# Kernel tuning notes

Measured on AMD Instinct MI355X. Metric: run time of the kernel, lower is better.

## Reference

```python
import jax, jax.numpy as jnp
import numpy as np

WIN = 9  # win_size from init

def setup_inputs() -> dict:
    key = jax.random.key(0)
    ks = jax.random.split(key, 4)
    N, L, C, U = 8, 4096, 256, 256
    x = jax.random.normal(ks[0], (N, L, C), dtype=jnp.float32)
    W_qry = jax.random.normal(ks[1], (C, U), dtype=jnp.float32) * 0.05
    W_key = jax.random.normal(ks[2], (C, U), dtype=jnp.float32) * 0.05
    v = jax.random.normal(ks[3], (U,), dtype=jnp.float32) * 0.05
    b = jnp.zeros((U,), dtype=jnp.float32)
    return {"x": x, "W_qry": W_qry, "W_key": W_key, "v": v, "b": b}

def reference(x, W_qry, W_key, v, b):
    N, L, C = x.shape
    n_w = L - WIN + 1
    # sliding-window gather: idx[w, s] = w + s
    idx = jnp.arange(n_w)[:, None] + jnp.arange(WIN)[None, :]
    x_win = x[:, idx]
    x_ctr = x[:, WIN // 2 : WIN // 2 + n_w]                    # [N, n_w, C]
    key = jnp.einsum('nwsc,cu->nwsu', x_win, W_key)
    qry = jnp.einsum('nwc,cu->nwu', x_ctr, W_qry)              # [N, n_w, U]
    score = jnp.einsum('nwsu,u->nws', jnp.tanh(qry[:, :, None, :] + key + b), v)
    weight = jax.nn.softmax(score, axis=2)                     # softmax over window dim
    out = jnp.einsum('nwsc,nws->nwc', x_win, weight)           # [N, n_w, C]
    return out
```

## Files before the change

kernel.cpp:

```cpp
#include <hip/hip_runtime.h>
#include <hip/hip_bf16.h>

#define WIN   9
#define NB    8
#define LL    4096
#define CC    256
#define UU    256
#define NW    (LL - WIN + 1)
#define MROWS (NB * LL)

#define BM 128
#define BK 64

typedef unsigned short ushort;
typedef __attribute__((ext_vector_type(8))) unsigned short ushort8v;
typedef __attribute__((ext_vector_type(4))) unsigned short ushort4v;
typedef __attribute__((ext_vector_type(8))) short short8v;
typedef __attribute__((ext_vector_type(4))) float f32x4;

__device__ __forceinline__ float bf16_to_f(ushort u) {
    return __uint_as_float(((unsigned int)u) << 16);
}
__device__ __forceinline__ ushort f2bf(float f) {
    __hip_bfloat16 h = __float2bfloat16(f);
    return *reinterpret_cast<ushort*>(&h);
}
__device__ __forceinline__ float fast_tanh(float x) {
    float e = __expf(2.0f * x);
    return 1.0f - 2.0f * __builtin_amdgcn_rcpf(e + 1.0f);
}

__global__ __launch_bounds__(256) void cvt_x(const float* __restrict__ X,
                                             ushort* __restrict__ Xb) {
    size_t i = ((size_t)blockIdx.x * 256 + threadIdx.x) * 8;
    float4 v0 = *reinterpret_cast<const float4*>(X + i);
    float4 v1 = *reinterpret_cast<const float4*>(X + i + 4);
    ushort8v o;
    o[0] = f2bf(v0.x); o[1] = f2bf(v0.y); o[2] = f2bf(v0.z); o[3] = f2bf(v0.w);
    o[4] = f2bf(v1.x); o[5] = f2bf(v1.y); o[6] = f2bf(v1.z); o[7] = f2bf(v1.w);
    *reinterpret_cast<ushort8v*>(Xb + i) = o;
}

__global__ __launch_bounds__(256) void transpose_w(const float* __restrict__ Wk,
                                                   const float* __restrict__ Wq,
                                                   ushort* __restrict__ WkT,
                                                   ushort* __restrict__ WqT) {
    const float* W = blockIdx.z ? Wq : Wk;
    ushort* O = blockIdx.z ? WqT : WkT;
    __shared__ float t[32][33];
    int c0 = blockIdx.x * 32, u0 = blockIdx.y * 32;
    int tr = threadIdx.x >> 3, tc = (threadIdx.x & 7) * 4;
    float4 v = *reinterpret_cast<const float4*>(&W[(size_t)(c0 + tr) * UU + u0 + tc]);
    t[tr][tc + 0] = v.x; t[tr][tc + 1] = v.y; t[tr][tc + 2] = v.z; t[tr][tc + 3] = v.w;
    __syncthreads();
    ushort4v o;
    #pragma unroll
    for (int i = 0; i < 4; ++i) o[i] = f2bf(t[tc + i][tr]);
    *reinterpret_cast<ushort4v*>(&O[(size_t)(u0 + tr) * CC + c0 + tc]) = o;
}

__global__ __launch_bounds__(256, 2) void gemm_lds(const ushort* __restrict__ Xb,
                                                   const ushort* __restrict__ WTall,
                                                   ushort* __restrict__ Kout,
                                                   ushort* __restrict__ Qout) {
    const int m0 = (blockIdx.x & 255) * BM;
    const int nt = blockIdx.x >> 8;
    const int n0 = nt * 128;

    __shared__ ushort As[2][BM * BK];
    __shared__ ushort Bs[2][BM * BK];

    const int tid = threadIdx.x;
    const int wid = tid >> 6, lane = tid & 63;
    const int wr = wid >> 1, wc = wid & 1;
    const int lrow = lane & 15;
    const int lkc  = lane >> 4;

    const int srow = wid * 8 + (lane >> 3);
    const int schunk = lane & 7;

    f32x4 acc[4][4] = {};

    auto stage = [&](int bi, int k0) {
        #pragma unroll
        for (int i = 0; i < 4; ++i) {
            int row = i * 32 + srow;
            int ca  = schunk ^ (row & 7);
            const ushort* srcA = Xb    + (size_t)(m0 + row) * CC + k0 + ca * 8;
            const ushort* srcB = WTall + (size_t)(n0 + row) * CC + k0 + ca * 8;
            ushort* dstA = &As[bi][i * 2048 + wid * 512];
            ushort* dstB = &Bs[bi][i * 2048 + wid * 512];
            __builtin_amdgcn_global_load_lds(
                (const __attribute__((address_space(1))) void*)srcA,
                (__attribute__((address_space(3))) void*)dstA, 16, 0, 0);
            __builtin_amdgcn_global_load_lds(
                (const __attribute__((address_space(1))) void*)srcB,
                (__attribute__((address_space(3))) void*)dstB, 16, 0, 0);
        }
    };

    stage(0, 0);
    __syncthreads();

    #pragma unroll
    for (int t = 0; t < 4; ++t) {
        const int cur = t & 1;
        if (t < 3) stage(cur ^ 1, (t + 1) * BK);

        #pragma unroll
        for (int ks = 0; ks < 2; ++ks) {
            short8v af[4], bq[4];
            #pragma unroll
            for (int m = 0; m < 4; ++m) {
                int r = wr * 64 + m * 16 + lrow;
                int cc = ks * 4 + lkc;
                af[m] = *reinterpret_cast<const short8v*>(&As[cur][r * 64 + (cc ^ (r & 7)) * 8]);
            }
            #pragma unroll
            for (int n = 0; n < 4; ++n) {
                int r = wc * 64 + n * 16 + lrow;
                int cc = ks * 4 + lkc;
                bq[n] = *reinterpret_cast<const short8v*>(&Bs[cur][r * 64 + (cc ^ (r & 7)) * 8]);
            }
            #pragma unroll
            for (int m = 0; m < 4; ++m)
                #pragma unroll
                for (int n = 0; n < 4; ++n)
                    acc[m][n] = __builtin_amdgcn_mfma_f32_16x16x32_bf16(af[m], bq[n], acc[m][n], 0, 0, 0);
        }
        if (t < 3) __syncthreads();
    }

    ushort* Out = (nt < 2) ? Kout : Qout;
    const int colbase = (nt & 1) * 128 + wc * 64;
    const int rowbase = m0 + wr * 64 + (lane >> 4) * 4;
    #pragma unroll
    for (int m = 0; m < 4; ++m)
        #pragma unroll
        for (int n = 0; n < 4; ++n)
            #pragma unroll
            for (int j = 0; j < 4; ++j)
                Out[(size_t)(rowbase + m * 16 + j) * UU + colbase + n * 16 + lrow] =
                    f2bf(acc[m][n][j]);
}

__global__ __launch_bounds__(256) void attn_smooth(
    const ushort* __restrict__ Xb,
    const ushort* __restrict__ Kb,
    const ushort* __restrict__ Qb,
    const float* __restrict__ v,
    const float* __restrict__ b,
    float* __restrict__ out) {
    const int wave = threadIdx.x >> 6;
    const int lane = threadIdx.x & 63;
    const int g = lane >> 4;
    const int t = lane & 15;
    const int bid = blockIdx.x;
    const int xcd = bid & 7, o8 = bid >> 3;
    const int nb = (xcd < 4 ? xcd * 256 : 1024 + (xcd - 4) * 255) + o8;
    const int item = nb * 16 + wave * 4 + g;
    const int n = item / NW;
    const int w = item - n * NW;
    const int u0 = t * 16;

    const size_t rowbase = (size_t)n * LL + w;

    float bb[16], vv[16];
    #pragma unroll
    for (int i = 0; i < 4; ++i) {
        *reinterpret_cast<float4*>(&bb[i * 4]) = *reinterpret_cast<const float4*>(b + u0 + i * 4);
        *reinterpret_cast<float4*>(&vv[i * 4]) = *reinterpret_cast<const float4*>(v + u0 + i * 4);
    }

    float qb[16];
    {
        const ushort* qrow = Qb + (rowbase + WIN / 2) * UU + u0;
        ushort8v q0 = *reinterpret_cast<const ushort8v*>(qrow);
        ushort8v q1 = *reinterpret_cast<const ushort8v*>(qrow + 8);
        #pragma unroll
        for (int i = 0; i < 8; ++i) {
            qb[i]     = bf16_to_f(q0[i]) + bb[i];
            qb[8 + i] = bf16_to_f(q1[i]) + bb[8 + i];
        }
    }

    float p[WIN];
    #pragma unroll
    for (int s = 0; s < WIN; ++s) {
        const ushort* krow = Kb + (rowbase + s) * UU + u0;
        ushort8v k0 = *reinterpret_cast<const ushort8v*>(krow);
        ushort8v k1 = *reinterpret_cast<const ushort8v*>(krow + 8);
        float a = 0.0f;
        #pragma unroll
        for (int i = 0; i < 8; ++i) {
            a += vv[i]     * fast_tanh(qb[i]     + bf16_to_f(k0[i]));
            a += vv[8 + i] * fast_tanh(qb[8 + i] + bf16_to_f(k1[i]));
        }
        p[s] = a;
    }
    #pragma unroll
    for (int off = 8; off; off >>= 1)
        #pragma unroll
        for (int s = 0; s < WIN; ++s)
            p[s] += __shfl_xor(p[s], off);

    float m = p[0];
    #pragma unroll
    for (int s = 1; s < WIN; ++s) m = fmaxf(m, p[s]);
    float e[WIN];
    float sum = 0.0f;
    #pragma unroll
    for (int s = 0; s < WIN; ++s) { e[s] = __expf(p[s] - m); sum += e[s]; }
    float inv = 1.0f / sum;

    float acc[16] = {};
    #pragma unroll
    for (int s = 0; s < WIN; ++s) {
        float ws = e[s] * inv;
        const ushort* xrow = Xb + (rowbase + s) * CC + u0;
        ushort8v x0 = *reinterpret_cast<const ushort8v*>(xrow);
        ushort8v x1 = *reinterpret_cast<const ushort8v*>(xrow + 8);
        #pragma unroll
        for (int i = 0; i < 8; ++i) {
            acc[i]     = fmaf(ws, bf16_to_f(x0[i]), acc[i]);
            acc[8 + i] = fmaf(ws, bf16_to_f(x1[i]), acc[8 + i]);
        }
    }
    float* orow = out + ((size_t)n * NW + w) * CC + u0;
    #pragma unroll
    for (int i = 0; i < 4; ++i)
        *reinterpret_cast<float4*>(orow + i * 4) = *reinterpret_cast<const float4*>(&acc[i * 4]);
}

extern "C" void kernel_launch(void* const* d_in, const int* in_sizes, int n_in,
                              void* d_out, int out_size, void* d_ws, size_t ws_size,
                              hipStream_t stream) {
    const float* x  = (const float*)d_in[0];
    const float* Wq = (const float*)d_in[1];
    const float* Wk = (const float*)d_in[2];
    const float* v  = (const float*)d_in[3];
    const float* b  = (const float*)d_in[4];
    float* out = (float*)d_out;

    const size_t MU = (size_t)MROWS * UU;
    ushort* Kbuf = (ushort*)d_ws;
    ushort* Qbuf = Kbuf + MU;
    ushort* Xb   = Qbuf + MU;
    ushort* WkT  = Xb + MU;
    ushort* WqT  = WkT + (size_t)CC * UU;

    cvt_x<<<MROWS * CC / (256 * 8), 256, 0, stream>>>(x, Xb);
    transpose_w<<<dim3(8, 8, 2), 256, 0, stream>>>(Wk, Wq, WkT, WqT);
    gemm_lds<<<1024, 256, 0, stream>>>(Xb, WkT, Kbuf, Qbuf);
    attn_smooth<<<2044, 256, 0, stream>>>(Xb, Kbuf, Qbuf, v, b, out);
}
```

Before: 136.0 us.

## Fuse x conversion, K/Q projection and windowed attention into one LDS-resident kernel

```diff
diff --git a/kernel.cpp b/kernel.cpp
--- a/kernel.cpp
+++ b/kernel.cpp
@@ -7,10 +7,9 @@
 #define CC    256
 #define UU    256
 #define NW    (LL - WIN + 1)
-#define MROWS (NB * LL)
-
-#define BM 128
-#define BK 64
+#define WB    56
+#define RB    64
+#define JB    73
 
 typedef unsigned short ushort;
 typedef __attribute__((ext_vector_type(8))) unsigned short ushort8v;
@@ -29,16 +28,8 @@
     float e = __expf(2.0f * x);
     return 1.0f - 2.0f * __builtin_amdgcn_rcpf(e + 1.0f);
 }
-
-__global__ __launch_bounds__(256) void cvt_x(const float* __restrict__ X,
-                                             ushort* __restrict__ Xb) {
-    size_t i = ((size_t)blockIdx.x * 256 + threadIdx.x) * 8;
-    float4 v0 = *reinterpret_cast<const float4*>(X + i);
-    float4 v1 = *reinterpret_cast<const float4*>(X + i + 4);
-    ushort8v o;
-    o[0] = f2bf(v0.x); o[1] = f2bf(v0.y); o[2] = f2bf(v0.z); o[3] = f2bf(v0.w);
-    o[4] = f2bf(v1.x); o[5] = f2bf(v1.y); o[6] = f2bf(v1.z); o[7] = f2bf(v1.w);
-    *reinterpret_cast<ushort8v*>(Xb + i) = o;
+__device__ __forceinline__ int SW(int c, int r) {
+    return (((c & 1) << 4) | (c >> 1)) ^ (r & 7);
 }
 
 __global__ __launch_bounds__(256) void transpose_w(const float* __restrict__ Wk,
@@ -59,177 +50,169 @@
     *reinterpret_cast<ushort4v*>(&O[(size_t)(u0 + tr) * CC + c0 + tc]) = o;
 }
 
-__global__ __launch_bounds__(256, 2) void gemm_lds(const ushort* __restrict__ Xb,
-                                                   const ushort* __restrict__ WTall,
-                                                   ushort* __restrict__ Kout,
-                                                   ushort* __restrict__ Qout) {
-    const int m0 = (blockIdx.x & 255) * BM;
-    const int nt = blockIdx.x >> 8;
-    const int n0 = nt * 128;
-
-    __shared__ ushort As[2][BM * BK];
-    __shared__ ushort Bs[2][BM * BK];
-
-    const int tid = threadIdx.x;
-    const int wid = tid >> 6, lane = tid & 63;
-    const int wr = wid >> 1, wc = wid & 1;
+__global__ __launch_bounds__(512, 1) void fused_smoother(
+    const float* __restrict__ X,
+    const ushort* __restrict__ WTall,
+    const float* __restrict__ v,
+    const float* __restrict__ b,
+    float* __restrict__ out)
+{
+    __shared__ ushort As[RB * CC];
+    __shared__ ushort Bs[64 * CC];
+    __shared__ ushort CK[RB * CC];
+    __shared__ ushort CQ[RB * CC];
+
+    const int bid = blockIdx.x;
+    const int n   = bid & 7;
+    const int j   = bid >> 3;
+    const int w0  = j * WB;
+
+    const int tid  = threadIdx.x;
+    const int wid  = tid >> 6;
+    const int lane = tid & 63;
+
+    const float* xbase = X + ((size_t)n * LL + w0) * CC;
+    #pragma unroll
+    for (int i = 0; i < 4; ++i) {
+        int cid = i * 512 + tid;
+        int row = cid >> 5, ch = cid & 31;
+        const float* src = xbase + row * CC + ch * 8;
+        float4 f0 = *reinterpret_cast<const float4*>(src);
+        float4 f1 = *reinterpret_cast<const float4*>(src + 4);
+        ushort8v o;
+        o[0] = f2bf(f0.x); o[1] = f2bf(f0.y); o[2] = f2bf(f0.z); o[3] = f2bf(f0.w);
+        o[4] = f2bf(f1.x); o[5] = f2bf(f1.y); o[6] = f2bf(f1.z); o[7] = f2bf(f1.w);
+        *reinterpret_cast<ushort8v*>(&As[row * CC + SW(ch, row) * 8]) = o;
+    }
+    __syncthreads();
+
+    const int m0w  = (wid & 3) * 16;
+    const int n0w  = (wid >> 2) * 32;
     const int lrow = lane & 15;
     const int lkc  = lane >> 4;
-
-    const int srow = wid * 8 + (lane >> 3);
-    const int schunk = lane & 7;
-
-    f32x4 acc[4][4] = {};
-
-    auto stage = [&](int bi, int k0) {
+    short8v af[8];
+    {
+        int r = m0w + lrow;
+        #pragma unroll
+        for (int k8 = 0; k8 < 8; ++k8) {
+            int cl = k8 * 4 + lkc;
+            af[k8] = *reinterpret_cast<const short8v*>(&As[r * CC + SW(cl, r) * 8]);
+        }
+    }
+
+    const int srow = tid >> 5;
+    (void)srow;
+    for (int s = 0; s < 8; ++s) {
+        if (s) __syncthreads();
+        const int s0 = s * 64;
         #pragma unroll
         for (int i = 0; i < 4; ++i) {
-            int row = i * 32 + srow;
-            int ca  = schunk ^ (row & 7);
-            const ushort* srcA = Xb    + (size_t)(m0 + row) * CC + k0 + ca * 8;
-            const ushort* srcB = WTall + (size_t)(n0 + row) * CC + k0 + ca * 8;
-            ushort* dstA = &As[bi][i * 2048 + wid * 512];
-            ushort* dstB = &Bs[bi][i * 2048 + wid * 512];
+            int gc = i * 512 + tid;
+            int row = gc >> 5, ch = gc & 31;
+            int ca  = ch ^ (row & 7);
+            const ushort* src = WTall + (size_t)(s0 + row) * CC + ca * 8;
+            ushort* dst = &Bs[(size_t)(i * 512 + wid * 64) * 8];
             __builtin_amdgcn_global_load_lds(
-                (const __attribute__((address_space(1))) void*)srcA,
-                (__attribute__((address_space(3))) void*)dstA, 16, 0, 0);
-            __builtin_amdgcn_global_load_lds(
-                (const __attribute__((address_space(1))) void*)srcB,
-                (__attribute__((address_space(3))) void*)dstB, 16, 0, 0);
-        }
-    };
-
-    stage(0, 0);
+                (const __attribute__((address_space(1))) void*)src,
+                (__attribute__((address_space(3))) void*)dst, 16, 0, 0);
+        }
+        __syncthreads();
+
+        f32x4 acc0 = {}, acc1 = {};
+        #pragma unroll
+        for (int k8 = 0; k8 < 8; ++k8) {
+            int cl  = k8 * 4 + lkc;
+            int rb0 = n0w + lrow;
+            int rb1 = n0w + 16 + lrow;
+            short8v b0 = *reinterpret_cast<const short8v*>(&Bs[rb0 * CC + ((cl ^ (rb0 & 7)) * 8)]);
+            short8v b1 = *reinterpret_cast<const short8v*>(&Bs[rb1 * CC + ((cl ^ (rb1 & 7)) * 8)]);
+            acc0 = __builtin_amdgcn_mfma_f32_16x16x32_bf16(af[k8], b0, acc0, 0, 0, 0);
+            acc1 = __builtin_amdgcn_mfma_f32_16x16x32_bf16(af[k8], b1, acc1, 0, 0, 0);
+        }
+        ushort* Cdst = (s0 + n0w < 256) ? CK : CQ;
+        const int colb = (s0 + n0w) & 255;
+        #pragma unroll
+        for (int nf = 0; nf < 2; ++nf) {
+            const f32x4 a = nf ? acc1 : acc0;
+            #pragma unroll
+            for (int jj = 0; jj < 4; ++jj) {
+                int rc  = m0w + (lane >> 4) * 4 + jj;
+                int col = colb + nf * 16 + lrow;
+                Cdst[rc * CC + SW(col >> 3, rc) * 8 + (col & 7)] = f2bf(a[jj]);
+            }
+        }
+    }
     __syncthreads();
 
-    #pragma unroll
-    for (int t = 0; t < 4; ++t) {
-        const int cur = t & 1;
-        if (t < 3) stage(cur ^ 1, (t + 1) * BK);
-
-        #pragma unroll
-        for (int ks = 0; ks < 2; ++ks) {
-            short8v af[4], bq[4];
-            #pragma unroll
-            for (int m = 0; m < 4; ++m) {
-                int r = wr * 64 + m * 16 + lrow;
-                int cc = ks * 4 + lkc;
-                af[m] = *reinterpret_cast<const short8v*>(&As[cur][r * 64 + (cc ^ (r & 7)) * 8]);
-            }
-            #pragma unroll
-            for (int n = 0; n < 4; ++n) {
-                int r = wc * 64 + n * 16 + lrow;
-                int cc = ks * 4 + lkc;
-                bq[n] = *reinterpret_cast<const short8v*>(&Bs[cur][r * 64 + (cc ^ (r & 7)) * 8]);
-            }
-            #pragma unroll
-            for (int m = 0; m < 4; ++m)
-                #pragma unroll
-                for (int n = 0; n < 4; ++n)
-                    acc[m][n] = __builtin_amdgcn_mfma_f32_16x16x32_bf16(af[m], bq[n], acc[m][n], 0, 0, 0);
-        }
-        if (t < 3) __syncthreads();
-    }
-
-    ushort* Out = (nt < 2) ? Kout : Qout;
-    const int colbase = (nt & 1) * 128 + wc * 64;
-    const int rowbase = m0 + wr * 64 + (lane >> 4) * 4;
-    #pragma unroll
-    for (int m = 0; m < 4; ++m)
-        #pragma unroll
-        for (int n = 0; n < 4; ++n)
-            #pragma unroll
-            for (int j = 0; j < 4; ++j)
-                Out[(size_t)(rowbase + m * 16 + j) * UU + colbase + n * 16 + lrow] =
-                    f2bf(acc[m][n][j]);
-}
-
-__global__ __launch_bounds__(256) void attn_smooth(
-    const ushort* __restrict__ Xb,
-    const ushort* __restrict__ Kb,
-    const ushort* __restrict__ Qb,
-    const float* __restrict__ v,
-    const float* __restrict__ b,
-    float* __restrict__ out) {
-    const int wave = threadIdx.x >> 6;
-    const int lane = threadIdx.x & 63;
-    const int g = lane >> 4;
-    const int t = lane & 15;
-    const int bid = blockIdx.x;
-    const int xcd = bid & 7, o8 = bid >> 3;
-    const int nb = (xcd < 4 ? xcd * 256 : 1024 + (xcd - 4) * 255) + o8;
-    const int item = nb * 16 + wave * 4 + g;
-    const int n = item / NW;
-    const int w = item - n * NW;
+    const int g = tid >> 4;
+    const int t = tid & 15;
     const int u0 = t * 16;
 
-    const size_t rowbase = (size_t)n * LL + w;
-
-    float bb[16], vv[16];
+    float vv[16], bb[16];
     #pragma unroll
     for (int i = 0; i < 4; ++i) {
+        *reinterpret_cast<float4*>(&vv[i * 4]) = *reinterpret_cast<const float4*>(v + u0 + i * 4);
         *reinterpret_cast<float4*>(&bb[i * 4]) = *reinterpret_cast<const float4*>(b + u0 + i * 4);
-        *reinterpret_cast<float4*>(&vv[i * 4]) = *reinterpret_cast<const float4*>(v + u0 + i * 4);
-    }
-
-    float qb[16];
-    {
-        const ushort* qrow = Qb + (rowbase + WIN / 2) * UU + u0;
-        ushort8v q0 = *reinterpret_cast<const ushort8v*>(qrow);
-        ushort8v q1 = *reinterpret_cast<const ushort8v*>(qrow + 8);
+    }
+
+    for (int wl = g; wl < WB; wl += 32) {
+        const int qr = wl + 4;
+        ushort8v q0 = *reinterpret_cast<const ushort8v*>(&CQ[qr * CC + SW(2 * t, qr) * 8]);
+        ushort8v q1 = *reinterpret_cast<const ushort8v*>(&CQ[qr * CC + SW(2 * t + 1, qr) * 8]);
+        float qb[16];
         #pragma unroll
         for (int i = 0; i < 8; ++i) {
             qb[i]     = bf16_to_f(q0[i]) + bb[i];
             qb[8 + i] = bf16_to_f(q1[i]) + bb[8 + i];
         }
-    }
-
-    float p[WIN];
-    #pragma unroll
-    for (int s = 0; s < WIN; ++s) {
-        const ushort* krow = Kb + (rowbase + s) * UU + u0;
-        ushort8v k0 = *reinterpret_cast<const ushort8v*>(krow);
-        ushort8v k1 = *reinterpret_cast<const ushort8v*>(krow + 8);
-        float a = 0.0f;
-        #pragma unroll
-        for (int i = 0; i < 8; ++i) {
-            a += vv[i]     * fast_tanh(qb[i]     + bf16_to_f(k0[i]));
-            a += vv[8 + i] * fast_tanh(qb[8 + i] + bf16_to_f(k1[i]));
-        }
-        p[s] = a;
-    }
-    #pragma unroll
-    for (int off = 8; off; off >>= 1)
-        #pragma unroll
-        for (int s = 0; s < WIN; ++s)
-            p[s] += __shfl_xor(p[s], off);
-
-    float m = p[0];
-    #pragma unroll
-    for (int s = 1; s < WIN; ++s) m = fmaxf(m, p[s]);
-    float e[WIN];
-    float sum = 0.0f;
-    #pragma unroll
-    for (int s = 0; s < WIN; ++s) { e[s] = __expf(p[s] - m); sum += e[s]; }
-    float inv = 1.0f / sum;
-
-    float acc[16] = {};
-    #pragma unroll
-    for (int s = 0; s < WIN; ++s) {
-        float ws = e[s] * inv;
-        const ushort* xrow = Xb + (rowbase + s) * CC + u0;
-        ushort8v x0 = *reinterpret_cast<const ushort8v*>(xrow);
-        ushort8v x1 = *reinterpret_cast<const ushort8v*>(xrow + 8);
-        #pragma unroll
-        for (int i = 0; i < 8; ++i) {
-            acc[i]     = fmaf(ws, bf16_to_f(x0[i]), acc[i]);
-            acc[8 + i] = fmaf(ws, bf16_to_f(x1[i]), acc[8 + i]);
-        }
-    }
-    float* orow = out + ((size_t)n * NW + w) * CC + u0;
-    #pragma unroll
-    for (int i = 0; i < 4; ++i)
-        *reinterpret_cast<float4*>(orow + i * 4) = *reinterpret_cast<const float4*>(&acc[i * 4]);
+
+        float p[WIN];
+        #pragma unroll
+        for (int s = 0; s < WIN; ++s) {
+            const int kr = wl + s;
+            ushort8v k0 = *reinterpret_cast<const ushort8v*>(&CK[kr * CC + SW(2 * t, kr) * 8]);
+            ushort8v k1 = *reinterpret_cast<const ushort8v*>(&CK[kr * CC + SW(2 * t + 1, kr) * 8]);
+            float a = 0.0f;
+            #pragma unroll
+            for (int i = 0; i < 8; ++i) {
+                a += vv[i]     * fast_tanh(qb[i]     + bf16_to_f(k0[i]));
+                a += vv[8 + i] * fast_tanh(qb[8 + i] + bf16_to_f(k1[i]));
+            }
+            p[s] = a;
+        }
+        #pragma unroll
+        for (int off = 8; off; off >>= 1)
+            #pragma unroll
+            for (int s = 0; s < WIN; ++s)
+                p[s] += __shfl_xor(p[s], off);
+
+        float m = p[0];
+        #pragma unroll
+        for (int s = 1; s < WIN; ++s) m = fmaxf(m, p[s]);
+        float e[WIN];
+        float sum = 0.0f;
+        #pragma unroll
+        for (int s = 0; s < WIN; ++s) { e[s] = __expf(p[s] - m); sum += e[s]; }
+        float inv = 1.0f / sum;
+
+        float acc[16] = {};
+        #pragma unroll
+        for (int s = 0; s < WIN; ++s) {
+            float ws = e[s] * inv;
+            const int ar = wl + s;
+            ushort8v x0 = *reinterpret_cast<const ushort8v*>(&As[ar * CC + SW(2 * t, ar) * 8]);
+            ushort8v x1 = *reinterpret_cast<const ushort8v*>(&As[ar * CC + SW(2 * t + 1, ar) * 8]);
+            #pragma unroll
+            for (int i = 0; i < 8; ++i) {
+                acc[i]     = fmaf(ws, bf16_to_f(x0[i]), acc[i]);
+                acc[8 + i] = fmaf(ws, bf16_to_f(x1[i]), acc[8 + i]);
+            }
+        }
+        float* orow = out + ((size_t)n * NW + w0 + wl) * CC + u0;
+        #pragma unroll
+        for (int i = 0; i < 4; ++i)
+            *reinterpret_cast<float4*>(orow + i * 4) = *reinterpret_cast<const float4*>(&acc[i * 4]);
+    }
 }
 
 extern "C" void kernel_launch(void* const* d_in, const int* in_sizes, int n_in,
@@ -242,15 +225,9 @@
     const float* b  = (const float*)d_in[4];
     float* out = (float*)d_out;
 
-    const size_t MU = (size_t)MROWS * UU;
-    ushort* Kbuf = (ushort*)d_ws;
-    ushort* Qbuf = Kbuf + MU;
-    ushort* Xb   = Qbuf + MU;
-    ushort* WkT  = Xb + MU;
-    ushort* WqT  = WkT + (size_t)CC * UU;
-
-    cvt_x<<<MROWS * CC / (256 * 8), 256, 0, stream>>>(x, Xb);
+    ushort* WkT = (ushort*)d_ws;
+    ushort* WqT = WkT + (size_t)CC * UU;
+
     transpose_w<<<dim3(8, 8, 2), 256, 0, stream>>>(Wk, Wq, WkT, WqT);
-    gemm_lds<<<1024, 256, 0, stream>>>(Xb, WkT, Kbuf, Qbuf);
-    attn_smooth<<<2044, 256, 0, stream>>>(Xb, Kbuf, Qbuf, v, b, out);
-}
+    fused_smoother<<<NB * JB, 512, 0, stream>>>(x, WkT, v, b, out);
+}
```

Result: slower. 159.5 us (+17.3%).
